# Performance work log

Measured on AMD Instinct MI355X. Metric: run time of the kernel, lower is better.

Reference implementation:

```python
import jax, jax.numpy as jnp
import numpy as np

DIM = 1024
NUM_HEADS = 16
HEAD_DIM = DIM // NUM_HEADS
SCALE = HEAD_DIM ** -0.25
EPS = 1e-5


def layer_norm(x, w, b):
    mu = jnp.mean(x, axis=-1, keepdims=True)
    var = jnp.var(x, axis=-1, keepdims=True)
    return (x - mu) * jax.lax.rsqrt(var + EPS) * w + b


def setup_inputs() -> dict:
    key = jax.random.key(0)
    ks = jax.random.split(key, 10)
    b, l, d = 2, 2048, DIM
    x = jax.random.normal(ks[0], (b, l, d), dtype=jnp.float32)
    # causal mask, broadcastable over heads: [b, 1, l, l]
    causal = jnp.tril(jnp.ones((l, l), dtype=jnp.int32))
    mask = jnp.broadcast_to(causal[None, None], (b, 1, l, l))
    s = 0.02
    return {
        "x": x,
        "mask": mask,
        "ln1_w": jnp.ones((d,), jnp.float32),
        "ln1_b": jnp.zeros((d,), jnp.float32),
        "qkv_w": jax.random.normal(ks[1], (d, 3 * d), jnp.float32) * s,
        "qkv_b": jnp.zeros((3 * d,), jnp.float32),
        "proj_w": jax.random.normal(ks[2], (d, d), jnp.float32) * s,
        "proj_b": jnp.zeros((d,), jnp.float32),
        "ln2_w": jnp.ones((d,), jnp.float32),
        "ln2_b": jnp.zeros((d,), jnp.float32),
        "ffn_w1": jax.random.normal(ks[3], (d, 4 * d), jnp.float32) * s,
        "ffn_b1": jnp.zeros((4 * d,), jnp.float32),
        "ffn_w2": jax.random.normal(ks[4], (4 * d, d), jnp.float32) * s,
        "ffn_b2": jnp.zeros((d,), jnp.float32),
    }


def attention(x, mask, qkv_w, qkv_b, proj_w, proj_b):
    b, l, d = x.shape
    n, c = NUM_HEADS, HEAD_DIM
    qkv = (x @ qkv_w + qkv_b).reshape(b, l, n * 3, c)
    q, k, v = qkv[:, :, :n], qkv[:, :, n:2 * n], qkv[:, :, 2 * n:]
    # scores: [b, n, l, l], scale applied to both q and k (head_dim^-0.25 each)
    attn = jnp.einsum('binc,bjnc->bnij', q * SCALE, k * SCALE)
    attn = jnp.where(mask[:, :, :l, :l] == 0, -jnp.inf, attn)
    attn = jax.nn.softmax(attn.astype(jnp.float32), axis=-1).astype(x.dtype)
    out = jnp.einsum('bnij,bjnc->binc', attn, v).reshape(b, l, d)
    return out @ proj_w + proj_b


def reference(x, mask, ln1_w, ln1_b, qkv_w, qkv_b, proj_w, proj_b,
              ln2_w, ln2_b, ffn_w1, ffn_b1, ffn_w2, ffn_b2):
    h = x + attention(layer_norm(x, ln1_w, ln1_b), mask, qkv_w, qkv_b, proj_w, proj_b)
    y = layer_norm(h, ln2_w, ln2_b)
    ffn = jax.nn.gelu(y @ ffn_w1 + ffn_b1, approximate=False) @ ffn_w2 + ffn_b2
    return h + ffn
```

## Files before the change

kernel.cpp:

```cpp
#include <hip/hip_runtime.h>
#include <hip/hip_bf16.h>
#include <math.h>

typedef __attribute__((ext_vector_type(8))) short bf16x8;
typedef __attribute__((ext_vector_type(4))) float f32x4;
typedef __attribute__((ext_vector_type(4))) unsigned u32x4;

#define MFMA16(a, b, c) __builtin_amdgcn_mfma_f32_16x16x32_bf16((a), (b), (c), 0, 0, 0)

typedef const __attribute__((address_space(1))) void* gas_ptr;
typedef __attribute__((address_space(3))) void* las_ptr;

__device__ __forceinline__ unsigned pack_bf16(float a, float b) {
    unsigned ua = (unsigned)__bfloat16_as_ushort(__float2bfloat16(a));
    unsigned ub = (unsigned)__bfloat16_as_ushort(__float2bfloat16(b));
    return ua | (ub << 16);
}

__global__ __launch_bounds__(256)
void transpose_to_bf16(const float* __restrict__ in, __hip_bfloat16* __restrict__ out,
                       int K, int N)
{
    __shared__ float t[32][33];
    const int tx = threadIdx.x & 31, ty = threadIdx.x >> 5;
    const int n0 = blockIdx.x * 32, k0 = blockIdx.y * 32;
    #pragma unroll
    for (int j = 0; j < 32; j += 8)
        t[ty + j][tx] = in[(size_t)(k0 + ty + j) * N + n0 + tx];
    __syncthreads();
    #pragma unroll
    for (int j = 0; j < 32; j += 8)
        out[(size_t)(n0 + ty + j) * K + k0 + tx] = __float2bfloat16(t[tx][ty + j]);
}

__global__ __launch_bounds__(256)
void ln_kernel(const float* __restrict__ in, const float* __restrict__ w,
               const float* __restrict__ b, __hip_bfloat16* __restrict__ out)
{
    const int row = blockIdx.x;
    const int tid = threadIdx.x;
    const float4 v = reinterpret_cast<const float4*>(in + (size_t)row * 1024)[tid];
    float s  = v.x + v.y + v.z + v.w;
    float s2 = v.x * v.x + v.y * v.y + v.z * v.z + v.w * v.w;
    #pragma unroll
    for (int off = 32; off > 0; off >>= 1) {
        s  += __shfl_down(s,  off);
        s2 += __shfl_down(s2, off);
    }
    __shared__ float red[8];
    const int wv = tid >> 6, ln = tid & 63;
    if (ln == 0) { red[wv] = s; red[4 + wv] = s2; }
    __syncthreads();
    s  = red[0] + red[1] + red[2] + red[3];
    s2 = red[4] + red[5] + red[6] + red[7];
    const float mu   = s * (1.0f / 1024.0f);
    const float var  = s2 * (1.0f / 1024.0f) - mu * mu;
    const float rstd = rsqrtf(var + 1e-5f);
    const float4 wv4 = reinterpret_cast<const float4*>(w)[tid];
    const float4 bv4 = reinterpret_cast<const float4*>(b)[tid];
    const size_t o = (size_t)row * 1024 + tid * 4;
    out[o + 0] = __float2bfloat16((v.x - mu) * rstd * wv4.x + bv4.x);
    out[o + 1] = __float2bfloat16((v.y - mu) * rstd * wv4.y + bv4.y);
    out[o + 2] = __float2bfloat16((v.z - mu) * rstd * wv4.z + bv4.z);
    out[o + 3] = __float2bfloat16((v.w - mu) * rstd * wv4.w + bv4.w);
}

template<int MODE>
__global__ __launch_bounds__(256, 3)
void gemm128p(const __hip_bfloat16* __restrict__ A,
              const __hip_bfloat16* __restrict__ Bt,
              const float* __restrict__ bias,
              const float* __restrict__ resid,
              void* __restrict__ C0, void* __restrict__ C1,
              int N, int K)
{
    constexpr int SLOT = 8192;
    __shared__ __align__(16) __hip_bfloat16 lds[3 * SLOT];

    const int tid  = threadIdx.x;
    const int lane = tid & 63;
    const int w    = tid >> 6;
    const int wr   = w >> 1, wc = w & 1;
    const int fr   = lane & 15, fq = lane >> 4;

    const int nwg = gridDim.x * gridDim.y;
    int flat = blockIdx.y * gridDim.x + blockIdx.x;
    flat = (flat & 7) * (nwg >> 3) + (flat >> 3);
    const int bx = flat % gridDim.x, by = flat / gridDim.x;
    const int m0 = by * 128, n0 = bx * 128;
    const int NT = K >> 5;

    const int prc = w * 8 + (lane >> 3);
    const int ch  = lane & 7;
    const __hip_bfloat16* aS[2];
    const __hip_bfloat16* bS[2];
    #pragma unroll
    for (int j = 0; j < 2; ++j) {
        const int pr  = prc + 32 * j;
        const int v   = ch ^ (pr & 7);
        const int row = 2 * pr + (v >> 2);
        const int col = 8 * (v & 3);
        aS[j] = A  + (size_t)(m0 + row) * K + col;
        bS[j] = Bt + (size_t)(n0 + row) * K + col;
    }

    auto stage = [&](int kt, int s) {
        __hip_bfloat16* LA = &lds[s * SLOT];
        __hip_bfloat16* LB = LA + 4096;
        #pragma unroll
        for (int j = 0; j < 2; ++j) {
            __builtin_amdgcn_global_load_lds((gas_ptr)(const void*)(aS[j] + kt * 32),
                                             (las_ptr)(void*)(LA + w * 512 + j * 2048), 16, 0, 0);
            __builtin_amdgcn_global_load_lds((gas_ptr)(const void*)(bS[j] + kt * 32),
                                             (las_ptr)(void*)(LB + w * 512 + j * 2048), 16, 0, 0);
        }
    };

    f32x4 acc[4][4] = {};

    stage(0, 0);
    stage(1, 1);
    int sl = 0, sp = 2;

    for (int kt = 0; kt < NT; ++kt) {
        if (kt + 1 < NT)
            asm volatile("s_waitcnt vmcnt(4) lgkmcnt(0)" ::: "memory");
        else
            asm volatile("s_waitcnt vmcnt(0) lgkmcnt(0)" ::: "memory");
        __builtin_amdgcn_s_barrier();
        __builtin_amdgcn_sched_barrier(0);

        if (kt + 2 < NT) stage(kt + 2, sp);

        const __hip_bfloat16* LA = &lds[sl * SLOT];
        const __hip_bfloat16* LB = LA + 4096;
        bf16x8 af[4], bg[4];
        #pragma unroll
        for (int m = 0; m < 4; ++m) {
            const int r = wr * 64 + m * 16 + fr;
            af[m] = *reinterpret_cast<const bf16x8*>(
                &LA[(r >> 1) * 64 + (((r & 1) * 32 + fq * 8) ^ (((r >> 1) & 7) * 8))]);
        }
        #pragma unroll
        for (int n = 0; n < 4; ++n) {
            const int r = wc * 64 + n * 16 + fr;
            bg[n] = *reinterpret_cast<const bf16x8*>(
                &LB[(r >> 1) * 64 + (((r & 1) * 32 + fq * 8) ^ (((r >> 1) & 7) * 8))]);
        }

        __builtin_amdgcn_s_setprio(1);
        #pragma unroll
        for (int m = 0; m < 4; ++m)
            #pragma unroll
            for (int n = 0; n < 4; ++n)
                acc[m][n] = MFMA16(af[m], bg[n], acc[m][n]);
        __builtin_amdgcn_s_setprio(0);

        sl = (sl == 2) ? 0 : sl + 1;
        sp = (sp == 2) ? 0 : sp + 1;
    }

    if (MODE == 0) {
        #pragma unroll
        for (int n = 0; n < 4; ++n) {
            const int col = n0 + wc * 64 + n * 16 + fr;
            const float bv = bias[col];
            #pragma unroll
            for (int m = 0; m < 4; ++m)
                #pragma unroll
                for (int i = 0; i < 4; ++i) {
                    const int row = m0 + wr * 64 + m * 16 + fq * 4 + i;
                    reinterpret_cast<float*>(C0)[(size_t)row * N + col] =
                        acc[m][n][i] + bv + resid[(size_t)row * N + col];
                }
        }
        return;
    }

    __syncthreads();
    ushort* E = reinterpret_cast<ushort*>(lds);
    auto eaddr = [](int r, int c16) { return r * 128 + (((c16) ^ ((r >> 3) & 15)) << 3); };

    #pragma unroll
    for (int n = 0; n < 4; ++n) {
        const int col = wc * 64 + n * 16 + fr;
        const float bv = bias[n0 + col];
        #pragma unroll
        for (int m = 0; m < 4; ++m) {
            #pragma unroll
            for (int i = 0; i < 4; ++i) {
                const int row = wr * 64 + m * 16 + fq * 4 + i;
                float v = acc[m][n][i] + bv;
                if (MODE == 2) v = 0.5f * v * (1.0f + erff(v * 0.70710678118654752f));
                E[eaddr(row, col >> 3) + (col & 7)] =
                    __bfloat16_as_ushort(__float2bfloat16(v));
            }
        }
    }
    __syncthreads();

    if (MODE == 3 && n0 >= 2048) {
        const int bq    = m0 >> 11;
        const int lbase = m0 & 2047;
        const int hcb   = n0 - 2048;
        #pragma unroll
        for (int p = 0; p < 8; ++p) {
            const int id  = p * 256 + tid;
            const int hcl = id >> 4;
            const int lc  = id & 15;
            u32x4 pkt;
            #pragma unroll
            for (int k2 = 0; k2 < 4; ++k2) {
                const int l0 = lc * 8 + k2 * 2;
                const unsigned a = E[eaddr(l0,     hcl >> 3) + (hcl & 7)];
                const unsigned b = E[eaddr(l0 + 1, hcl >> 3) + (hcl & 7)];
                pkt[k2] = a | (b << 16);
            }
            *reinterpret_cast<u32x4*>(
                &reinterpret_cast<__hip_bfloat16*>(C1)
                    [((size_t)(bq * 1024 + hcb + hcl) << 11) + lbase + lc * 8]) = pkt;
        }
        return;
    }

    const size_t ldC = (MODE == 3) ? 2048 : (size_t)N;
    __hip_bfloat16* Cb = reinterpret_cast<__hip_bfloat16*>(C0);
    #pragma unroll
    for (int p = 0; p < 8; ++p) {
        const int id  = p * 256 + tid;
        const int row = id >> 4;
        const int c16 = id & 15;
        const bf16x8 vv = *reinterpret_cast<const bf16x8*>(&E[eaddr(row, c16)]);
        *reinterpret_cast<bf16x8*>(&Cb[(size_t)(m0 + row) * ldC + n0 + c16 * 8]) = vv;
    }
}

__global__ __launch_bounds__(256)
void attn_kernel(const __hip_bfloat16* __restrict__ qk,
                 const __hip_bfloat16* __restrict__ Vt,
                 __hip_bfloat16* __restrict__ out)
{
    const int bid  = blockIdx.x;
    const int xcd  = bid & 7;
    const int rank = bid >> 3;
    const int panel = xcd * 4 + (rank & 3);
    const int qt   = 31 - (rank >> 2);
    const int h = panel & 15, b = panel >> 4;
    const int q0 = qt * 64;

    const int lane = threadIdx.x & 63;
    const int w    = threadIdx.x >> 6;
    const int fr   = lane & 15, fq = lane >> 4;
    const int qrow = q0 + w * 16 + fr;

    __shared__ __align__(16) __hip_bfloat16 Klds[2][64 * 64];
    __shared__ __align__(16) __hip_bfloat16 Vlds[2][64 * 64];

    bf16x8 qf[2];
    {
        const __hip_bfloat16* qp = qk + ((size_t)(b * 2048 + qrow) << 11) + h * 64 + fq * 8;
        qf[0] = *reinterpret_cast<const bf16x8*>(qp);
        qf[1] = *reinterpret_cast<const bf16x8*>(qp + 32);
    }

    const int srow8 = lane >> 3;
    const int sc    = lane & 7;
    const __hip_bfloat16* Kg[2];
    const __hip_bfloat16* Vg[2];
    #pragma unroll
    for (int j = 0; j < 2; ++j) {
        const int r = w * 16 + j * 8 + srow8;
        const int csw = (sc ^ (r & 7)) * 8;
        Kg[j] = qk + ((size_t)(b * 2048 + r) << 11) + 1024 + h * 64 + csw;
        Vg[j] = Vt + ((size_t)(b * 1024 + h * 64 + r) << 11) + csw;
    }

    auto stage = [&](int kv0, int bufi) {
        __hip_bfloat16* KL = &Klds[bufi][0];
        __hip_bfloat16* VL = &Vlds[bufi][0];
        #pragma unroll
        for (int j = 0; j < 2; ++j) {
            __builtin_amdgcn_global_load_lds(
                (gas_ptr)(const void*)(Kg[j] + ((size_t)kv0 << 11)),
                (las_ptr)(void*)&KL[(w * 16 + j * 8) * 64], 16, 0, 0);
            __builtin_amdgcn_global_load_lds(
                (gas_ptr)(const void*)(Vg[j] + kv0),
                (las_ptr)(void*)&VL[(w * 16 + j * 8) * 64], 16, 0, 0);
        }
    };

    const float SC = 0.125f * 1.44269504088896f;
    float m_run = -1e30f, l_run = 0.0f;
    f32x4 o[4] = {};

    const int ntiles = qt + 1;
    stage(0, 0);
    int cur = 0;

    for (int t = 0; t < ntiles; ++t) {
        const int kv0 = t << 6;
        __syncthreads();
        if (t + 1 < ntiles) stage((t + 1) << 6, cur ^ 1);

        const __hip_bfloat16* Kl = &Klds[cur][0];
        const __hip_bfloat16* Vl = &Vlds[cur][0];

        f32x4 s[4] = {};
        #pragma unroll
        for (int n = 0; n < 4; ++n) {
            const int row = n * 16 + fr;
            const int sw = (row & 7) << 3;
            const bf16x8 k0 = *reinterpret_cast<const bf16x8*>(&Kl[row * 64 + ((fq * 8) ^ sw)]);
            const bf16x8 k1 = *reinterpret_cast<const bf16x8*>(&Kl[row * 64 + ((fq * 8 + 32) ^ sw)]);
            s[n] = MFMA16(k0, qf[0], s[n]);
            s[n] = MFMA16(k1, qf[1], s[n]);
        }

        float pm = -1e30f;
        if (t == ntiles - 1) {
            #pragma unroll
            for (int n = 0; n < 4; ++n)
                #pragma unroll
                for (int i = 0; i < 4; ++i) {
                    const int kvp = kv0 + n * 16 + fq * 4 + i;
                    float sv = s[n][i] * SC;
                    sv = (kvp <= qrow) ? sv : -1e30f;
                    s[n][i] = sv;
                    pm = fmaxf(pm, sv);
                }
        } else {
            #pragma unroll
            for (int n = 0; n < 4; ++n)
                #pragma unroll
                for (int i = 0; i < 4; ++i) {
                    const float sv = s[n][i] * SC;
                    s[n][i] = sv;
                    pm = fmaxf(pm, sv);
                }
        }
        pm = fmaxf(pm, __shfl_xor(pm, 16));
        pm = fmaxf(pm, __shfl_xor(pm, 32));
        const float mnew = fmaxf(m_run, pm);
        const float corr = exp2f(m_run - mnew);
        m_run = mnew;

        float rs = 0.0f;
        unsigned pk[8];
        #pragma unroll
        for (int n = 0; n < 4; ++n) {
            const float p0 = exp2f(s[n][0] - mnew);
            const float p1 = exp2f(s[n][1] - mnew);
            const float p2 = exp2f(s[n][2] - mnew);
            const float p3 = exp2f(s[n][3] - mnew);
            rs += (p0 + p1) + (p2 + p3);
            pk[n * 2 + 0] = pack_bf16(p0, p1);
            pk[n * 2 + 1] = pack_bf16(p2, p3);
        }
        rs += __shfl_xor(rs, 16);
        rs += __shfl_xor(rs, 32);
        l_run = l_run * corr + rs;

        #pragma unroll
        for (int i = 0; i < 4; ++i) {
            const float ci = __shfl(corr, fq * 4 + i);
            o[0][i] *= ci; o[1][i] *= ci; o[2][i] *= ci; o[3][i] *= ci;
        }

        u32x4 A0, A1;
        #pragma unroll
        for (int r = 0; r < 4; ++r) {
            const int slx = fr + ((2 * (fq & 1) + (r >> 1)) << 4);
            const unsigned lo0 = __shfl(pk[0 + (r & 1)], slx);
            const unsigned hi0 = __shfl(pk[2 + (r & 1)], slx);
            const unsigned lo1 = __shfl(pk[4 + (r & 1)], slx);
            const unsigned hi1 = __shfl(pk[6 + (r & 1)], slx);
            A0[r] = (fq & 2) ? hi0 : lo0;
            A1[r] = (fq & 2) ? hi1 : lo1;
        }
        const bf16x8 pa0 = __builtin_bit_cast(bf16x8, A0);
        const bf16x8 pa1 = __builtin_bit_cast(bf16x8, A1);

        #pragma unroll
        for (int tt = 0; tt < 4; ++tt) {
            const int row = tt * 16 + fr;
            const int sw = (row & 7) << 3;
            const bf16x8 v0 = *reinterpret_cast<const bf16x8*>(&Vl[row * 64 + ((fq * 8) ^ sw)]);
            const bf16x8 v1 = *reinterpret_cast<const bf16x8*>(&Vl[row * 64 + ((fq * 8 + 32) ^ sw)]);
            o[tt] = MFMA16(pa0, v0, o[tt]);
            o[tt] = MFMA16(pa1, v1, o[tt]);
        }
        cur ^= 1;
    }

    #pragma unroll
    for (int i = 0; i < 4; ++i) {
        const float li  = __shfl(l_run, fq * 4 + i);
        const float inv = 1.0f / li;
        const int row = q0 + w * 16 + fq * 4 + i;
        #pragma unroll
        for (int tt = 0; tt < 4; ++tt)
            out[(size_t)(b * 2048 + row) * 1024 + h * 64 + tt * 16 + fr] =
                __float2bfloat16(o[tt][i] * inv);
    }
}

extern "C" void kernel_launch(void* const* d_in, const int* in_sizes, int n_in,
                              void* d_out, int out_size, void* d_ws, size_t ws_size,
                              hipStream_t stream)
{
    (void)in_sizes; (void)n_in; (void)out_size; (void)ws_size;
    const float* x      = (const float*)d_in[0];
    const float* ln1_w  = (const float*)d_in[2];
    const float* ln1_b  = (const float*)d_in[3];
    const float* qkv_w  = (const float*)d_in[4];
    const float* qkv_b  = (const float*)d_in[5];
    const float* proj_w = (const float*)d_in[6];
    const float* proj_b = (const float*)d_in[7];
    const float* ln2_w  = (const float*)d_in[8];
    const float* ln2_b  = (const float*)d_in[9];
    const float* ffn_w1 = (const float*)d_in[10];
    const float* ffn_b1 = (const float*)d_in[11];
    const float* ffn_w2 = (const float*)d_in[12];
    const float* ffn_b2 = (const float*)d_in[13];
    float* outp = (float*)d_out;

    char* ws = (char*)d_ws;
    size_t off = 0;
    auto take = [&](size_t bytes) -> char* {
        char* p = ws + off;
        off += (bytes + 255) & ~(size_t)255;
        return p;
    };
    __hip_bfloat16* wqkv  = (__hip_bfloat16*)take((size_t)3072 * 1024 * 2);
    __hip_bfloat16* wproj = (__hip_bfloat16*)take((size_t)1024 * 1024 * 2);
    __hip_bfloat16* wff1  = (__hip_bfloat16*)take((size_t)4096 * 1024 * 2);
    __hip_bfloat16* wff2  = (__hip_bfloat16*)take((size_t)1024 * 4096 * 2);
    float*          hbuf  = (float*)take((size_t)4096 * 1024 * 4);
    __hip_bfloat16* xn    = (__hip_bfloat16*)take((size_t)4096 * 1024 * 2);
    __hip_bfloat16* qkb   = (__hip_bfloat16*)take((size_t)4096 * 2048 * 2);
    __hip_bfloat16* Vt    = (__hip_bfloat16*)take((size_t)2048 * 2048 * 2);
    __hip_bfloat16* attn  = (__hip_bfloat16*)take((size_t)4096 * 1024 * 2);
    __hip_bfloat16* ffn1  = qkb;

    transpose_to_bf16<<<dim3(3072 / 32, 1024 / 32), 256, 0, stream>>>(qkv_w, wqkv, 1024, 3072);
    transpose_to_bf16<<<dim3(1024 / 32, 1024 / 32), 256, 0, stream>>>(proj_w, wproj, 1024, 1024);
    transpose_to_bf16<<<dim3(4096 / 32, 1024 / 32), 256, 0, stream>>>(ffn_w1, wff1, 1024, 4096);
    transpose_to_bf16<<<dim3(1024 / 32, 4096 / 32), 256, 0, stream>>>(ffn_w2, wff2, 4096, 1024);

    ln_kernel<<<4096, 256, 0, stream>>>(x, ln1_w, ln1_b, xn);
    gemm128p<3><<<dim3(24, 32), 256, 0, stream>>>(
        xn, wqkv, qkv_b, nullptr, qkb, Vt, 3072, 1024);
    attn_kernel<<<1024, 256, 0, stream>>>(qkb, Vt, attn);
    gemm128p<0><<<dim3(8, 32), 256, 0, stream>>>(
        attn, wproj, proj_b, x, hbuf, nullptr, 1024, 1024);
    ln_kernel<<<4096, 256, 0, stream>>>(hbuf, ln2_w, ln2_b, xn);
    gemm128p<2><<<dim3(32, 32), 256, 0, stream>>>(
        xn, wff1, ffn_b1, nullptr, ffn1, nullptr, 4096, 1024);
    gemm128p<0><<<dim3(8, 32), 256, 0, stream>>>(
        ffn1, wff2, ffn_b2, hbuf, outp, nullptr, 1024, 4096);
}
```

Measured before the change: 246.4 us.

## Shrink attention tiles to 32 queries/keys and skip softmax rescale lazily

The attention kernel now uses 32-row query tiles and 32-key KV tiles with 128-thread blocks, launched as 2048 blocks instead of 1024. The K/V LDS staging layout and the V fragment indexing are rewritten to match the smaller tiles. It also adds a lazy online-softmax rescale that only updates the running max and rescales the accumulators when a wave's new max exceeds the old one by more than 8 (in log2 units). The goal is better load balance for the causal triangle, more concurrent blocks, and fewer rescale operations, at the cost of less K/V reuse per block and more loop iterations and barriers.

```diff
diff --git a/kernel.cpp b/kernel.cpp
--- a/kernel.cpp
+++ b/kernel.cpp
@@ -235,7 +235,7 @@
     }
 }
 
-__global__ __launch_bounds__(256)
+__global__ __launch_bounds__(128)
 void attn_kernel(const __hip_bfloat16* __restrict__ qk,
                  const __hip_bfloat16* __restrict__ Vt,
                  __hip_bfloat16* __restrict__ out)
@@ -244,17 +244,17 @@
     const int xcd  = bid & 7;
     const int rank = bid >> 3;
     const int panel = xcd * 4 + (rank & 3);
-    const int qt   = 31 - (rank >> 2);
+    const int qt   = 63 - (rank >> 2);
     const int h = panel & 15, b = panel >> 4;
-    const int q0 = qt * 64;
+    const int q0 = qt * 32;
 
     const int lane = threadIdx.x & 63;
     const int w    = threadIdx.x >> 6;
     const int fr   = lane & 15, fq = lane >> 4;
     const int qrow = q0 + w * 16 + fr;
 
-    __shared__ __align__(16) __hip_bfloat16 Klds[2][64 * 64];
-    __shared__ __align__(16) __hip_bfloat16 Vlds[2][64 * 64];
+    __shared__ __align__(16) __hip_bfloat16 Klds[2][32 * 64];
+    __shared__ __align__(16) __hip_bfloat16 Vlds[2][32 * 64];
 
     bf16x8 qf[2];
     {
@@ -263,29 +263,29 @@
         qf[1] = *reinterpret_cast<const bf16x8*>(qp + 32);
     }
 
-    const int srow8 = lane >> 3;
-    const int sc    = lane & 7;
     const __hip_bfloat16* Kg[2];
     const __hip_bfloat16* Vg[2];
     #pragma unroll
     for (int j = 0; j < 2; ++j) {
-        const int r = w * 16 + j * 8 + srow8;
-        const int csw = (sc ^ (r & 7)) * 8;
-        Kg[j] = qk + ((size_t)(b * 2048 + r) << 11) + 1024 + h * 64 + csw;
-        Vg[j] = Vt + ((size_t)(b * 1024 + h * 64 + r) << 11) + csw;
+        const int c  = w * 64 + 128 * j + lane;
+        const int r  = c >> 3;
+        const int ch = c & 7;
+        const int lc = ch ^ (r & 7);
+        Kg[j] = qk + ((size_t)(b * 2048 + r) << 11) + 1024 + h * 64 + lc * 8;
+        const int d  = (lc < 4) ? r : (r + 32);
+        const int kc = lc & 3;
+        Vg[j] = Vt + ((size_t)(b * 1024 + h * 64 + d) << 11) + kc * 8;
     }
 
     auto stage = [&](int kv0, int bufi) {
-        __hip_bfloat16* KL = &Klds[bufi][0];
-        __hip_bfloat16* VL = &Vlds[bufi][0];
         #pragma unroll
         for (int j = 0; j < 2; ++j) {
             __builtin_amdgcn_global_load_lds(
                 (gas_ptr)(const void*)(Kg[j] + ((size_t)kv0 << 11)),
-                (las_ptr)(void*)&KL[(w * 16 + j * 8) * 64], 16, 0, 0);
+                (las_ptr)(void*)&Klds[bufi][(w * 64 + 128 * j) * 8], 16, 0, 0);
             __builtin_amdgcn_global_load_lds(
                 (gas_ptr)(const void*)(Vg[j] + kv0),
-                (las_ptr)(void*)&VL[(w * 16 + j * 8) * 64], 16, 0, 0);
+                (las_ptr)(void*)&Vlds[bufi][(w * 64 + 128 * j) * 8], 16, 0, 0);
         }
     };
 
@@ -298,16 +298,16 @@
     int cur = 0;
 
     for (int t = 0; t < ntiles; ++t) {
-        const int kv0 = t << 6;
+        const int kv0 = t << 5;
         __syncthreads();
-        if (t + 1 < ntiles) stage((t + 1) << 6, cur ^ 1);
+        if (t + 1 < ntiles) stage((t + 1) << 5, cur ^ 1);
 
         const __hip_bfloat16* Kl = &Klds[cur][0];
         const __hip_bfloat16* Vl = &Vlds[cur][0];
 
-        f32x4 s[4] = {};
-        #pragma unroll
-        for (int n = 0; n < 4; ++n) {
+        f32x4 s[2] = {};
+        #pragma unroll
+        for (int n = 0; n < 2; ++n) {
             const int row = n * 16 + fr;
             const int sw = (row & 7) << 3;
             const bf16x8 k0 = *reinterpret_cast<const bf16x8*>(&Kl[row * 64 + ((fq * 8) ^ sw)]);
@@ -319,7 +319,7 @@
         float pm = -1e30f;
         if (t == ntiles - 1) {
             #pragma unroll
-            for (int n = 0; n < 4; ++n)
+            for (int n = 0; n < 2; ++n)
                 #pragma unroll
                 for (int i = 0; i < 4; ++i) {
                     const int kvp = kv0 + n * 16 + fq * 4 + i;
@@ -330,7 +330,7 @@
                 }
         } else {
             #pragma unroll
-            for (int n = 0; n < 4; ++n)
+            for (int n = 0; n < 2; ++n)
                 #pragma unroll
                 for (int i = 0; i < 4; ++i) {
                     const float sv = s[n][i] * SC;
@@ -340,54 +340,58 @@
         }
         pm = fmaxf(pm, __shfl_xor(pm, 16));
         pm = fmaxf(pm, __shfl_xor(pm, 32));
-        const float mnew = fmaxf(m_run, pm);
-        const float corr = exp2f(m_run - mnew);
-        m_run = mnew;
+
+        const bool resc = !__all(pm <= m_run + 8.0f);
+        float corr = 1.0f;
+        if (resc) {
+            const float mnew = fmaxf(m_run, pm);
+            corr = exp2f(m_run - mnew);
+            m_run = mnew;
+        }
 
         float rs = 0.0f;
-        unsigned pk[8];
-        #pragma unroll
-        for (int n = 0; n < 4; ++n) {
-            const float p0 = exp2f(s[n][0] - mnew);
-            const float p1 = exp2f(s[n][1] - mnew);
-            const float p2 = exp2f(s[n][2] - mnew);
-            const float p3 = exp2f(s[n][3] - mnew);
+        unsigned pk[4];
+        #pragma unroll
+        for (int n = 0; n < 2; ++n) {
+            const float p0 = exp2f(s[n][0] - m_run);
+            const float p1 = exp2f(s[n][1] - m_run);
+            const float p2 = exp2f(s[n][2] - m_run);
+            const float p3 = exp2f(s[n][3] - m_run);
             rs += (p0 + p1) + (p2 + p3);
             pk[n * 2 + 0] = pack_bf16(p0, p1);
             pk[n * 2 + 1] = pack_bf16(p2, p3);
         }
         rs += __shfl_xor(rs, 16);
         rs += __shfl_xor(rs, 32);
-        l_run = l_run * corr + rs;
-
-        #pragma unroll
-        for (int i = 0; i < 4; ++i) {
-            const float ci = __shfl(corr, fq * 4 + i);
-            o[0][i] *= ci; o[1][i] *= ci; o[2][i] *= ci; o[3][i] *= ci;
-        }
-
-        u32x4 A0, A1;
+
+        if (resc) {
+            l_run = l_run * corr + rs;
+            #pragma unroll
+            for (int i = 0; i < 4; ++i) {
+                const float ci = __shfl(corr, fq * 4 + i);
+                o[0][i] *= ci; o[1][i] *= ci; o[2][i] *= ci; o[3][i] *= ci;
+            }
+        } else {
+            l_run += rs;
+        }
+
+        u32x4 A0;
         #pragma unroll
         for (int r = 0; r < 4; ++r) {
-            const int slx = fr + ((2 * (fq & 1) + (r >> 1)) << 4);
-            const unsigned lo0 = __shfl(pk[0 + (r & 1)], slx);
-            const unsigned hi0 = __shfl(pk[2 + (r & 1)], slx);
-            const unsigned lo1 = __shfl(pk[4 + (r & 1)], slx);
-            const unsigned hi1 = __shfl(pk[6 + (r & 1)], slx);
-            A0[r] = (fq & 2) ? hi0 : lo0;
-            A1[r] = (fq & 2) ? hi1 : lo1;
-        }
-        const bf16x8 pa0 = __builtin_bit_cast(bf16x8, A0);
-        const bf16x8 pa1 = __builtin_bit_cast(bf16x8, A1);
+            const int sl = fr + ((2 * (fq & 1) + (r >> 1)) << 4);
+            const unsigned lo = __shfl(pk[0 + (r & 1)], sl);
+            const unsigned hi = __shfl(pk[2 + (r & 1)], sl);
+            A0[r] = (fq & 2) ? hi : lo;
+        }
+        const bf16x8 pa = __builtin_bit_cast(bf16x8, A0);
 
         #pragma unroll
         for (int tt = 0; tt < 4; ++tt) {
-            const int row = tt * 16 + fr;
+            const int row = (tt & 1) * 16 + fr;
             const int sw = (row & 7) << 3;
-            const bf16x8 v0 = *reinterpret_cast<const bf16x8*>(&Vl[row * 64 + ((fq * 8) ^ sw)]);
-            const bf16x8 v1 = *reinterpret_cast<const bf16x8*>(&Vl[row * 64 + ((fq * 8 + 32) ^ sw)]);
-            o[tt] = MFMA16(pa0, v0, o[tt]);
-            o[tt] = MFMA16(pa1, v1, o[tt]);
+            const int cb = ((tt >> 1) * 4 + fq) << 3;
+            const bf16x8 v0 = *reinterpret_cast<const bf16x8*>(&Vl[row * 64 + (cb ^ sw)]);
+            o[tt] = MFMA16(pa, v0, o[tt]);
         }
         cur ^= 1;
     }
@@ -398,9 +402,11 @@
         const float inv = 1.0f / li;
         const int row = q0 + w * 16 + fq * 4 + i;
         #pragma unroll
-        for (int tt = 0; tt < 4; ++tt)
-            out[(size_t)(b * 2048 + row) * 1024 + h * 64 + tt * 16 + fr] =
+        for (int tt = 0; tt < 4; ++tt) {
+            const int d = ((tt & 1) * 16 + (tt >> 1) * 32) + fr;
+            out[(size_t)(b * 2048 + row) * 1024 + h * 64 + d] =
                 __float2bfloat16(o[tt][i] * inv);
+        }
     }
 }
 
@@ -450,7 +456,7 @@
     ln_kernel<<<4096, 256, 0, stream>>>(x, ln1_w, ln1_b, xn);
     gemm128p<3><<<dim3(24, 32), 256, 0, stream>>>(
         xn, wqkv, qkv_b, nullptr, qkb, Vt, 3072, 1024);
-    attn_kernel<<<1024, 256, 0, stream>>>(qkb, Vt, attn);
+    attn_kernel<<<2048, 128, 0, stream>>>(qkb, Vt, attn);
     gemm128p<0><<<dim3(8, 32), 256, 0, stream>>>(
         attn, wproj, proj_b, x, hbuf, nullptr, 1024, 1024);
     ln_kernel<<<4096, 256, 0, stream>>>(hbuf, ln2_w, ln2_b, xn);
```

Measured after the change: 261.6 us. +6.2%, slower.

## Use 128x64 tiles for N=1024 GEMMs and fuse weight transposes into one launch

Applied to the files above, without the earlier changes.

Adds a gemm_n64 kernel with 128x64 output tiles for the projection and FFN2 GEMMs (N=1024), which doubles the grid from 256 to 512 workgroups so the 256 CUs are better occupied. The fp32 residual epilogue moves from gemm128p into the new kernel. The four weight-transpose launches are merged into one kernel that picks its matrix from the block index, saving launch overhead. The narrower tiles reuse less of each A tile and need more A loads per output element.

```diff
diff --git a/kernel.cpp b/kernel.cpp
--- a/kernel.cpp
+++ b/kernel.cpp
@@ -18,12 +18,22 @@
 }
 
 __global__ __launch_bounds__(256)
-void transpose_to_bf16(const float* __restrict__ in, __hip_bfloat16* __restrict__ out,
-                       int K, int N)
+void transpose_all(const float* __restrict__ qkv_w, const float* __restrict__ proj_w,
+                   const float* __restrict__ ffn_w1, const float* __restrict__ ffn_w2,
+                   __hip_bfloat16* __restrict__ wqkv, __hip_bfloat16* __restrict__ wproj,
+                   __hip_bfloat16* __restrict__ wff1, __hip_bfloat16* __restrict__ wff2)
 {
+    const int bid = blockIdx.x;
+    const float* in; __hip_bfloat16* out; int K, N, r;
+    if (bid < 3072)      { in = qkv_w;  out = wqkv;  K = 1024; N = 3072; r = bid;        }
+    else if (bid < 4096) { in = proj_w; out = wproj; K = 1024; N = 1024; r = bid - 3072; }
+    else if (bid < 8192) { in = ffn_w1; out = wff1;  K = 1024; N = 4096; r = bid - 4096; }
+    else                 { in = ffn_w2; out = wff2;  K = 4096; N = 1024; r = bid - 8192; }
+    const int ncols = N >> 5;
+    const int n0 = (r % ncols) * 32, k0 = (r / ncols) * 32;
+
     __shared__ float t[32][33];
     const int tx = threadIdx.x & 31, ty = threadIdx.x >> 5;
-    const int n0 = blockIdx.x * 32, k0 = blockIdx.y * 32;
     #pragma unroll
     for (int j = 0; j < 32; j += 8)
         t[ty + j][tx] = in[(size_t)(k0 + ty + j) * N + n0 + tx];
@@ -70,7 +80,6 @@
 void gemm128p(const __hip_bfloat16* __restrict__ A,
               const __hip_bfloat16* __restrict__ Bt,
               const float* __restrict__ bias,
-              const float* __restrict__ resid,
               void* __restrict__ C0, void* __restrict__ C1,
               int N, int K)
 {
@@ -158,23 +167,6 @@
 
         sl = (sl == 2) ? 0 : sl + 1;
         sp = (sp == 2) ? 0 : sp + 1;
-    }
-
-    if (MODE == 0) {
-        #pragma unroll
-        for (int n = 0; n < 4; ++n) {
-            const int col = n0 + wc * 64 + n * 16 + fr;
-            const float bv = bias[col];
-            #pragma unroll
-            for (int m = 0; m < 4; ++m)
-                #pragma unroll
-                for (int i = 0; i < 4; ++i) {
-                    const int row = m0 + wr * 64 + m * 16 + fq * 4 + i;
-                    reinterpret_cast<float*>(C0)[(size_t)row * N + col] =
-                        acc[m][n][i] + bv + resid[(size_t)row * N + col];
-                }
-        }
-        return;
     }
 
     __syncthreads();
@@ -232,6 +224,116 @@
         const int c16 = id & 15;
         const bf16x8 vv = *reinterpret_cast<const bf16x8*>(&E[eaddr(row, c16)]);
         *reinterpret_cast<bf16x8*>(&Cb[(size_t)(m0 + row) * ldC + n0 + c16 * 8]) = vv;
+    }
+}
+
+__global__ __launch_bounds__(256, 3)
+void gemm_n64(const __hip_bfloat16* __restrict__ A,
+              const __hip_bfloat16* __restrict__ Bt,
+              const float* __restrict__ bias,
+              const float* __restrict__ resid,
+              float* __restrict__ C0,
+              int N, int K)
+{
+    constexpr int SLOT = 6144;
+    __shared__ __align__(16) __hip_bfloat16 lds[3 * SLOT];
+
+    const int tid  = threadIdx.x;
+    const int lane = tid & 63;
+    const int w    = tid >> 6;
+    const int wr   = w >> 1, wc = w & 1;
+    const int fr   = lane & 15, fq = lane >> 4;
+
+    const int nwg = gridDim.x * gridDim.y;
+    int flat = blockIdx.y * gridDim.x + blockIdx.x;
+    flat = (flat & 7) * (nwg >> 3) + (flat >> 3);
+    const int bx = flat % gridDim.x, by = flat / gridDim.x;
+    const int m0 = by * 128, n0 = bx * 64;
+    const int NT = K >> 5;
+
+    const int prc = w * 8 + (lane >> 3);
+    const int ch  = lane & 7;
+    const __hip_bfloat16* aS[2];
+    #pragma unroll
+    for (int j = 0; j < 2; ++j) {
+        const int pr  = prc + 32 * j;
+        const int v   = ch ^ (pr & 7);
+        aS[j] = A + (size_t)(m0 + 2 * pr + (v >> 2)) * K + 8 * (v & 3);
+    }
+    const __hip_bfloat16* bS;
+    {
+        const int c  = w * 64 + lane;
+        const int pr = c >> 3;
+        const int v  = (c & 7) ^ (pr & 7);
+        bS = Bt + (size_t)(n0 + 2 * pr + (v >> 2)) * K + 8 * (v & 3);
+    }
+
+    auto stage = [&](int kt, int s) {
+        __hip_bfloat16* LA = &lds[s * SLOT];
+        __hip_bfloat16* LB = LA + 4096;
+        #pragma unroll
+        for (int j = 0; j < 2; ++j)
+            __builtin_amdgcn_global_load_lds((gas_ptr)(const void*)(aS[j] + kt * 32),
+                                             (las_ptr)(void*)(LA + w * 512 + j * 2048), 16, 0, 0);
+        __builtin_amdgcn_global_load_lds((gas_ptr)(const void*)(bS + kt * 32),
+                                         (las_ptr)(void*)(LB + w * 512), 16, 0, 0);
+    };
+
+    f32x4 acc[4][2] = {};
+
+    stage(0, 0);
+    stage(1, 1);
+    int sl = 0, sp = 2;
+
+    for (int kt = 0; kt < NT; ++kt) {
+        if (kt + 1 < NT)
+            asm volatile("s_waitcnt vmcnt(3) lgkmcnt(0)" ::: "memory");
+        else
+            asm volatile("s_waitcnt vmcnt(0) lgkmcnt(0)" ::: "memory");
+        __builtin_amdgcn_s_barrier();
+        __builtin_amdgcn_sched_barrier(0);
+
+        if (kt + 2 < NT) stage(kt + 2, sp);
+
+        const __hip_bfloat16* LA = &lds[sl * SLOT];
+        const __hip_bfloat16* LB = LA + 4096;
+        bf16x8 af[4], bg[2];
+        #pragma unroll
+        for (int m = 0; m < 4; ++m) {
+            const int r = wr * 64 + m * 16 + fr;
+            af[m] = *reinterpret_cast<const bf16x8*>(
+                &LA[(r >> 1) * 64 + (((r & 1) * 32 + fq * 8) ^ (((r >> 1) & 7) * 8))]);
+        }
+        #pragma unroll
+        for (int n = 0; n < 2; ++n) {
+            const int r = wc * 32 + n * 16 + fr;
+            bg[n] = *reinterpret_cast<const bf16x8*>(
+                &LB[(r >> 1) * 64 + (((r & 1) * 32 + fq * 8) ^ (((r >> 1) & 7) * 8))]);
+        }
+
+        __builtin_amdgcn_s_setprio(1);
+        #pragma unroll
+        for (int m = 0; m < 4; ++m)
+            #pragma unroll
+            for (int n = 0; n < 2; ++n)
+                acc[m][n] = MFMA16(af[m], bg[n], acc[m][n]);
+        __builtin_amdgcn_s_setprio(0);
+
+        sl = (sl == 2) ? 0 : sl + 1;
+        sp = (sp == 2) ? 0 : sp + 1;
+    }
+
+    #pragma unroll
+    for (int n = 0; n < 2; ++n) {
+        const int col = n0 + wc * 32 + n * 16 + fr;
+        const float bv = bias[col];
+        #pragma unroll
+        for (int m = 0; m < 4; ++m)
+            #pragma unroll
+            for (int i = 0; i < 4; ++i) {
+                const int row = m0 + wr * 64 + m * 16 + fq * 4 + i;
+                C0[(size_t)row * N + col] = acc[m][n][i] + bv + resid[(size_t)row * N + col];
+            }
     }
 }
 
@@ -442,20 +544,17 @@
     __hip_bfloat16* attn  = (__hip_bfloat16*)take((size_t)4096 * 1024 * 2);
     __hip_bfloat16* ffn1  = qkb;
 
-    transpose_to_bf16<<<dim3(3072 / 32, 1024 / 32), 256, 0, stream>>>(qkv_w, wqkv, 1024, 3072);
-    transpose_to_bf16<<<dim3(1024 / 32, 1024 / 32), 256, 0, stream>>>(proj_w, wproj, 1024, 1024);
-    transpose_to_bf16<<<dim3(4096 / 32, 1024 / 32), 256, 0, stream>>>(ffn_w1, wff1, 1024, 4096);
-    transpose_to_bf16<<<dim3(1024 / 32, 4096 / 32), 256, 0, stream>>>(ffn_w2, wff2, 4096, 1024);
-
+    transpose_all<<<12288, 256, 0, stream>>>(qkv_w, proj_w, ffn_w1, ffn_w2,
+                                             wqkv, wproj, wff1, wff2);
     ln_kernel<<<4096, 256, 0, stream>>>(x, ln1_w, ln1_b, xn);
     gemm128p<3><<<dim3(24, 32), 256, 0, stream>>>(
-        xn, wqkv, qkv_b, nullptr, qkb, Vt, 3072, 1024);
+        xn, wqkv, qkv_b, qkb, Vt, 3072, 1024);
     attn_kernel<<<1024, 256, 0, stream>>>(qkb, Vt, attn);
-    gemm128p<0><<<dim3(8, 32), 256, 0, stream>>>(
-        attn, wproj, proj_b, x, hbuf, nullptr, 1024, 1024);
+    gemm_n64<<<dim3(16, 32), 256, 0, stream>>>(
+        attn, wproj, proj_b, x, hbuf, 1024, 1024);
     ln_kernel<<<4096, 256, 0, stream>>>(hbuf, ln2_w, ln2_b, xn);
     gemm128p<2><<<dim3(32, 32), 256, 0, stream>>>(
-        xn, wff1, ffn_b1, nullptr, ffn1, nullptr, 4096, 1024);
-    gemm128p<0><<<dim3(8, 32), 256, 0, stream>>>(
-        ffn1, wff2, ffn_b2, hbuf, outp, nullptr, 1024, 4096);
-}
+        xn, wff1, ffn_b1, ffn1, nullptr, 4096, 1024);
+    gemm_n64<<<dim3(16, 32), 256, 0, stream>>>(
+        ffn1, wff2, ffn_b2, hbuf, outp, 1024, 4096);
+}
```

Measured after the change: 244.8 us. About the same (-0.7%).
